# Kernel tuning notes

Hardware: AMD Instinct MI355X
Metric: run time of the kernel (lower is better)

Reference implementation:

```python
import jax, jax.numpy as jnp
import numpy as np
from jax import lax

NUM_CLASSES = 5  # config['training']['num_classes_per_task']
EMBED_DIM = 64


def _conv(x, w, b, pad):
    y = lax.conv_general_dilated(x, w, (1, 1), [(pad, pad), (pad, pad)],
                                 dimension_numbers=('NCHW', 'OIHW', 'NCHW'))
    return y + b[None, :, None, None]


def _maxpool2(x):
    n, c, h, w = x.shape
    return x.reshape(n, c, h // 2, 2, w // 2, 2).max(axis=(3, 5))


def _lenet(x, c1w, c1b, c2w, c2b, f1w, f1b, f2w, f2b, f3w, f3b):
    h = _maxpool2(jax.nn.relu(_conv(x, c1w, c1b, pad=2)))   # [N,6,14,14]
    h = _maxpool2(jax.nn.relu(_conv(h, c2w, c2b, pad=0)))   # [N,16,5,5]
    h = h.reshape(h.shape[0], -1)                            # [N,400]
    h = jax.nn.relu(h @ f1w.T + f1b)                         # [N,120]
    h = jax.nn.relu(h @ f2w.T + f2b)                         # [N,84]
    return h @ f3w.T + f3b                                   # [N,64]


def setup_inputs() -> dict:
    key = jax.random.key(0)
    ks = jax.random.split(key, 12)
    s = 0.1
    return {
        'x': jax.random.normal(ks[0], (20480, 1, 28, 28), dtype=jnp.float32),
        'c1w': jax.random.normal(ks[1], (6, 1, 5, 5), dtype=jnp.float32) * s,
        'c1b': jnp.zeros((6,), dtype=jnp.float32),
        'c2w': jax.random.normal(ks[2], (16, 6, 5, 5), dtype=jnp.float32) * s,
        'c2b': jnp.zeros((16,), dtype=jnp.float32),
        'f1w': jax.random.normal(ks[3], (120, 400), dtype=jnp.float32) * s,
        'f1b': jnp.zeros((120,), dtype=jnp.float32),
        'f2w': jax.random.normal(ks[4], (84, 120), dtype=jnp.float32) * s,
        'f2b': jnp.zeros((84,), dtype=jnp.float32),
        'f3w': jax.random.normal(ks[5], (EMBED_DIM, 84), dtype=jnp.float32) * s,
        'f3b': jnp.zeros((EMBED_DIM,), dtype=jnp.float32),
    }


def reference(x, c1w, c1b, c2w, c2b, f1w, f1b, f2w, f2b, f3w, f3b):
    emb = _lenet(x, c1w, c1b, c2w, c2b, f1w, f1b, f2w, f2b, f3w, f3b)  # [N,D]
    # Source builds a flat prototypes list of all N*D scalars / num_classes,
    # but only indices 0..D-1 are ever read -> first embedding row / num_classes.
    proto = emb[0] / NUM_CLASSES                     # [D]
    s = jax.nn.softmax(emb, axis=1)                  # softmax over dim 1
    # fun_L(x, p) = sqrt((x-p)^2) = |x-p|
    logits = jnp.abs(s - proto[None, :])             # [N,D]
    batch_size = x.shape[0] // NUM_CLASSES
    return logits.reshape(batch_size, NUM_CLASSES, -1)
```

## Files before the change

### kernel.cpp

```cpp
#include <hip/hip_runtime.h>


__device__ __forceinline__ int xcd_swizzle(int orig, int nwg) {
    int xcd = orig & 7, q = nwg >> 3, r = nwg & 7;
    int base = (xcd < r) ? xcd * (q + 1) : r * (q + 1) + (xcd - r) * q;
    return base + (orig >> 3);
}

__global__ __launch_bounds__(256) void transpose_x(
    const float* __restrict__ x, float* __restrict__ xt, int nc)
{
    __shared__ float t[64][65];
    const int tx = threadIdx.x & 63, ty = threadIdx.x >> 6;
    const int p0 = blockIdx.x * 64, n0 = blockIdx.y * 64;
    #pragma unroll
    for (int rr = 0; rr < 16; ++rr) {
        int nl = rr * 4 + ty;
        int pp = p0 + tx;
        int pr = pp >> 5, pc = pp & 31;
        float v = 0.f;
        if (pr >= 2 && pr < 30 && pc >= 2 && pc < 30)
            v = x[(size_t)(n0 + nl) * 784 + (pr - 2) * 28 + (pc - 2)];
        t[tx][nl] = v;
    }
    __syncthreads();
    #pragma unroll
    for (int rr = 0; rr < 16; ++rr) {
        int pl = rr * 4 + ty;
        xt[(size_t)(p0 + pl) * nc + n0 + tx] = t[pl][tx];
    }
}

__global__ __launch_bounds__(256, 2) void conv1_bt(
    const float* __restrict__ xt, const float* __restrict__ c1w,
    const float* __restrict__ c1b, float* __restrict__ p1t, int nc)
{
    const int newid = xcd_swizzle(blockIdx.x, gridDim.x);
    const int grp = newid / 392, rem = newid - grp * 392;
    const int pass = rem / 196, pos = rem - pass * 196;
    const int py = pos / 14, px = pos - py * 14;
    const int img = grp * 512 + threadIdx.x * 2;
    const float* pb = xt + (size_t)((2 * py) * 32 + 2 * px) * nc + img;

    float2 acc[12];
    #pragma unroll
    for (int i = 0; i < 12; ++i) acc[i] = make_float2(0.f, 0.f);

    #pragma unroll
    for (int r = 0; r < 6; ++r) {
        float2 row[6];
        #pragma unroll
        for (int cc = 0; cc < 6; ++cc)
            row[cc] = *(const float2*)&pb[(size_t)(r * 32 + cc) * nc];
        #pragma unroll
        for (int c3 = 0; c3 < 3; ++c3) {
            const float* wp = c1w + (pass * 3 + c3) * 25;
            if (r <= 4) {
                #pragma unroll
                for (int kx = 0; kx < 5; ++kx) {
                    float w = wp[r * 5 + kx];
                    acc[c3*4+0].x += row[kx].x   * w;
                    acc[c3*4+0].y += row[kx].y   * w;
                    acc[c3*4+1].x += row[kx+1].x * w;
                    acc[c3*4+1].y += row[kx+1].y * w;
                }
            }
            if (r >= 1) {
                #pragma unroll
                for (int kx = 0; kx < 5; ++kx) {
                    float w = wp[(r - 1) * 5 + kx];
                    acc[c3*4+2].x += row[kx].x   * w;
                    acc[c3*4+2].y += row[kx].y   * w;
                    acc[c3*4+3].x += row[kx+1].x * w;
                    acc[c3*4+3].y += row[kx+1].y * w;
                }
            }
        }
    }
    #pragma unroll
    for (int c3 = 0; c3 < 3; ++c3) {
        int ch = pass * 3 + c3;
        float b = c1b[ch];
        float mx = fmaxf(fmaxf(acc[c3*4+0].x, acc[c3*4+1].x),
                         fmaxf(acc[c3*4+2].x, acc[c3*4+3].x)) + b;
        float my = fmaxf(fmaxf(acc[c3*4+0].y, acc[c3*4+1].y),
                         fmaxf(acc[c3*4+2].y, acc[c3*4+3].y)) + b;
        float2 o2 = make_float2(fmaxf(mx, 0.f), fmaxf(my, 0.f));
        *(float2*)&p1t[(size_t)(ch * 196 + pos) * nc + img] = o2;
    }
}

__global__ __launch_bounds__(256, 2) void conv2_bt(
    const float* __restrict__ p1t, const float* __restrict__ c2w,
    const float* __restrict__ c2b, float* __restrict__ ht, int nc)
{
    const int newid = xcd_swizzle(blockIdx.x, gridDim.x);
    const int grp = newid / 100, rem = newid - grp * 100;
    const int pass = rem / 25, pos = rem - pass * 25;
    const int qy = pos / 5, qx = pos - qy * 5;
    const int img = grp * 512 + threadIdx.x * 2;
    const int y0 = 2 * qy, x0 = 2 * qx;

    float2 acc[16];
    #pragma unroll
    for (int i = 0; i < 16; ++i) acc[i] = make_float2(0.f, 0.f);

    #pragma unroll 1
    for (int ci = 0; ci < 6; ++ci) {
        const float* pb = p1t + (size_t)(ci * 196 + y0 * 14 + x0) * nc + img;
        #pragma unroll
        for (int r = 0; r < 6; ++r) {
            float2 row[6];
            #pragma unroll
            for (int cc = 0; cc < 6; ++cc)
                row[cc] = *(const float2*)&pb[(size_t)(r * 14 + cc) * nc];
            #pragma unroll
            for (int o4 = 0; o4 < 4; ++o4) {
                const float* wp = c2w + ((pass * 4 + o4) * 6 + ci) * 25;
                if (r <= 4) {
                    #pragma unroll
                    for (int kx = 0; kx < 5; ++kx) {
                        float w = wp[r * 5 + kx];
                        acc[o4*4+0].x += row[kx].x   * w;
                        acc[o4*4+0].y += row[kx].y   * w;
                        acc[o4*4+1].x += row[kx+1].x * w;
                        acc[o4*4+1].y += row[kx+1].y * w;
                    }
                }
                if (r >= 1) {
                    #pragma unroll
                    for (int kx = 0; kx < 5; ++kx) {
                        float w = wp[(r - 1) * 5 + kx];
                        acc[o4*4+2].x += row[kx].x   * w;
                        acc[o4*4+2].y += row[kx].y   * w;
                        acc[o4*4+3].x += row[kx+1].x * w;
                        acc[o4*4+3].y += row[kx+1].y * w;
                    }
                }
            }
        }
    }
    #pragma unroll
    for (int o4 = 0; o4 < 4; ++o4) {
        int oc = pass * 4 + o4;
        float b = c2b[oc];
        float mx = fmaxf(fmaxf(acc[o4*4+0].x, acc[o4*4+1].x),
                         fmaxf(acc[o4*4+2].x, acc[o4*4+3].x)) + b;
        float my = fmaxf(fmaxf(acc[o4*4+0].y, acc[o4*4+1].y),
                         fmaxf(acc[o4*4+2].y, acc[o4*4+3].y)) + b;
        float2 o2 = make_float2(fmaxf(mx, 0.f), fmaxf(my, 0.f));
        *(float2*)&ht[(size_t)(oc * 25 + pos) * nc + img] = o2;
    }
}

__global__ __launch_bounds__(256) void fc1_bt(
    const float* __restrict__ ht, const float* __restrict__ f1w,
    const float* __restrict__ f1b, float* __restrict__ a1t, int nc)
{
    const int newid = xcd_swizzle(blockIdx.x, gridDim.x);
    const int grp = newid / 15, og = newid - grp * 15;
    const int img = grp * 512 + threadIdx.x * 2;
    const float* wb = f1w + og * 8 * 400;

    float2 acc[8];
    #pragma unroll
    for (int j = 0; j < 8; ++j) acc[j] = make_float2(0.f, 0.f);

    #pragma unroll 4
    for (int k = 0; k < 400; ++k) {
        float2 hv = *(const float2*)&ht[(size_t)k * nc + img];
        #pragma unroll
        for (int j = 0; j < 8; ++j) {
            float w = wb[j * 400 + k];
            acc[j].x += hv.x * w;
            acc[j].y += hv.y * w;
        }
    }
    #pragma unroll
    for (int j = 0; j < 8; ++j) {
        int o = og * 8 + j;
        float b = f1b[o];
        float2 o2 = make_float2(fmaxf(acc[j].x + b, 0.f),
                                fmaxf(acc[j].y + b, 0.f));
        *(float2*)&a1t[(size_t)o * nc + img] = o2;
    }
}

__global__ __launch_bounds__(256) void fc2_bt(
    const float* __restrict__ a1t, const float* __restrict__ f2w,
    const float* __restrict__ f2b, float* __restrict__ a2t, int nc)
{
    const int newid = xcd_swizzle(blockIdx.x, gridDim.x);
    const int grp = newid / 12, og = newid - grp * 12;
    const int img = grp * 512 + threadIdx.x * 2;
    const float* wb = f2w + og * 7 * 120;

    float2 acc[7];
    #pragma unroll
    for (int j = 0; j < 7; ++j) acc[j] = make_float2(0.f, 0.f);

    #pragma unroll 4
    for (int k = 0; k < 120; ++k) {
        float2 hv = *(const float2*)&a1t[(size_t)k * nc + img];
        #pragma unroll
        for (int j = 0; j < 7; ++j) {
            float w = wb[j * 120 + k];
            acc[j].x += hv.x * w;
            acc[j].y += hv.y * w;
        }
    }
    #pragma unroll
    for (int j = 0; j < 7; ++j) {
        int o = og * 7 + j;
        float b = f2b[o];
        float2 o2 = make_float2(fmaxf(acc[j].x + b, 0.f),
                                fmaxf(acc[j].y + b, 0.f));
        *(float2*)&a2t[(size_t)o * nc + img] = o2;
    }
}

__global__ __launch_bounds__(256) void fc3_bt(
    const float* __restrict__ a2t, const float* __restrict__ f3w,
    const float* __restrict__ f3b, float* __restrict__ embt,
    int nc, int Ntot, int n0)
{
    const int newid = xcd_swizzle(blockIdx.x, gridDim.x);
    const int grp = newid / 8, og = newid - grp * 8;
    const int limg = grp * 512 + threadIdx.x * 2;
    const float* wb = f3w + og * 8 * 84;

    float2 acc[8];
    #pragma unroll
    for (int j = 0; j < 8; ++j) acc[j] = make_float2(0.f, 0.f);

    #pragma unroll 4
    for (int k = 0; k < 84; ++k) {
        float2 hv = *(const float2*)&a2t[(size_t)k * nc + limg];
        #pragma unroll
        for (int j = 0; j < 8; ++j) {
            float w = wb[j * 84 + k];
            acc[j].x += hv.x * w;
            acc[j].y += hv.y * w;
        }
    }
    #pragma unroll
    for (int j = 0; j < 8; ++j) {
        int o = og * 8 + j;
        float b = f3b[o];
        float2 o2 = make_float2(acc[j].x + b, acc[j].y + b);
        *(float2*)&embt[(size_t)o * Ntot + n0 + limg] = o2;
    }
}

__global__ __launch_bounds__(256) void proto_head_t(
    const float* __restrict__ embt, float* __restrict__ out, int N)
{
    const int img = blockIdx.x * 256 + threadIdx.x;
    float v[64];
    float m = -1e30f;
    #pragma unroll
    for (int o = 0; o < 64; ++o) {
        v[o] = embt[(size_t)o * N + img];
        m = fmaxf(m, v[o]);
    }
    float s = 0.f;
    #pragma unroll
    for (int o = 0; o < 64; ++o) {
        v[o] = __expf(v[o] - m);
        s += v[o];
    }
    float inv = __frcp_rn(s);
    #pragma unroll
    for (int o = 0; o < 64; o += 4) {
        float4 r;
        r.x = fabsf(v[o+0] * inv - embt[(size_t)(o+0) * N] * 0.2f);
        r.y = fabsf(v[o+1] * inv - embt[(size_t)(o+1) * N] * 0.2f);
        r.z = fabsf(v[o+2] * inv - embt[(size_t)(o+2) * N] * 0.2f);
        r.w = fabsf(v[o+3] * inv - embt[(size_t)(o+3) * N] * 0.2f);
        *(float4*)&out[(size_t)img * 64 + o] = r;
    }
}

extern "C" void kernel_launch(void* const* d_in, const int* in_sizes, int n_in,
                              void* d_out, int out_size, void* d_ws, size_t ws_size,
                              hipStream_t stream)
{
    const float* x   = (const float*)d_in[0];
    const float* c1w = (const float*)d_in[1];
    const float* c1b = (const float*)d_in[2];
    const float* c2w = (const float*)d_in[3];
    const float* c2b = (const float*)d_in[4];
    const float* f1w = (const float*)d_in[5];
    const float* f1b = (const float*)d_in[6];
    const float* f2w = (const float*)d_in[7];
    const float* f2b = (const float*)d_in[8];
    const float* f3w = (const float*)d_in[9];
    const float* f3b = (const float*)d_in[10];
    float* out = (float*)d_out;

    const int N = in_sizes[0] / 784;
    float* base = (float*)d_ws;

    int c = 40;
    const int cands[] = {1, 2, 4, 5, 8, 10, 20, 40};
    for (int k = 0; k < 8; ++k) {
        int cd = cands[k];
        if (N % cd) continue;
        int ncq = N / cd;
        if (ncq % 512) continue;
        size_t need = (size_t)8800 * ncq + (size_t)256 * N;
        if (need <= ws_size) { c = cd; break; }
    }
    const int nc = N / c;

    float* xt   = base;
    float* p1t  = base + (size_t)1024 * nc;
    float* ht_  = base;
    float* a1t  = p1t;
    float* a2t  = p1t + (size_t)120 * nc;
    float* embt = base + (size_t)2200 * nc;

    for (int k = 0; k < c; ++k) {
        int n0 = k * nc;
        transpose_x<<<dim3(16, nc / 64), 256, 0, stream>>>(
            x + (size_t)n0 * 784, xt, nc);
        conv1_bt<<<392 * (nc / 512), 256, 0, stream>>>(
            xt, c1w, c1b, p1t, nc);
        conv2_bt<<<100 * (nc / 512), 256, 0, stream>>>(
            p1t, c2w, c2b, ht_, nc);
        fc1_bt<<<15 * (nc / 512), 256, 0, stream>>>(
            ht_, f1w, f1b, a1t, nc);
        fc2_bt<<<12 * (nc / 512), 256, 0, stream>>>(
            a1t, f2w, f2b, a2t, nc);
        fc3_bt<<<8 * (nc / 512), 256, 0, stream>>>(
            a2t, f3w, f3b, embt, nc, N, n0);
    }
    proto_head_t<<<N / 256, 256, 0, stream>>>(embt, out, N);
}
```

Measured before the change: 299.4 us.

## Run conv2 on bf16 MFMA with hi/lo split-precision packing of activations

Conv1 now writes its output as packed bf16 hi/lo pairs in one 32-bit word per value. Conv2 is rewritten as an implicit GEMM on 16x16x32 bf16 MFMA instructions, using three products (hi*hi, hi*lo, lo*hi) to recover near-fp32 accuracy. The aim is to move conv2's scalar FMA work onto the matrix cores. In exchange, the B operand is gathered with scattered 32-bit loads per lane, and the result carries a small precision risk compared with fp32.

```diff
diff --git a/kernel.cpp b/kernel.cpp
--- a/kernel.cpp
+++ b/kernel.cpp
@@ -1,10 +1,22 @@
 #include <hip/hip_runtime.h>
 
+
+typedef __attribute__((ext_vector_type(8))) short bf16x8;
+typedef __attribute__((ext_vector_type(4))) float f32x4;
+
+union PackB { uint32_t u[4]; bf16x8 v; };
 
 __device__ __forceinline__ int xcd_swizzle(int orig, int nwg) {
     int xcd = orig & 7, q = nwg >> 3, r = nwg & 7;
     int base = (xcd < r) ? xcd * (q + 1) : r * (q + 1) + (xcd - r) * q;
     return base + (orig >> 3);
+}
+
+__device__ __forceinline__ uint32_t pack_hilo(float v) {
+    uint32_t u = __float_as_uint(v);
+    uint32_t hb = u & 0xFFFF0000u;
+    float lo = v - __uint_as_float(hb);
+    return hb | (__float_as_uint(lo) >> 16);
 }
 
 __global__ __launch_bounds__(256) void transpose_x(
@@ -33,7 +45,7 @@
 
 __global__ __launch_bounds__(256, 2) void conv1_bt(
     const float* __restrict__ xt, const float* __restrict__ c1w,
-    const float* __restrict__ c1b, float* __restrict__ p1t, int nc)
+    const float* __restrict__ c1b, uint32_t* __restrict__ p1p, int nc)
 {
     const int newid = xcd_swizzle(blockIdx.x, gridDim.x);
     const int grp = newid / 392, rem = newid - grp * 392;
@@ -85,71 +97,97 @@
                          fmaxf(acc[c3*4+2].x, acc[c3*4+3].x)) + b;
         float my = fmaxf(fmaxf(acc[c3*4+0].y, acc[c3*4+1].y),
                          fmaxf(acc[c3*4+2].y, acc[c3*4+3].y)) + b;
-        float2 o2 = make_float2(fmaxf(mx, 0.f), fmaxf(my, 0.f));
-        *(float2*)&p1t[(size_t)(ch * 196 + pos) * nc + img] = o2;
-    }
-}
-
-__global__ __launch_bounds__(256, 2) void conv2_bt(
-    const float* __restrict__ p1t, const float* __restrict__ c2w,
+        uint2 o2;
+        o2.x = pack_hilo(fmaxf(mx, 0.f));
+        o2.y = pack_hilo(fmaxf(my, 0.f));
+        *(uint2*)&p1p[(size_t)(ch * 196 + pos) * nc + img] = o2;
+    }
+}
+
+__global__ __launch_bounds__(256) void conv2_mfma(
+    const uint32_t* __restrict__ p1p, const float* __restrict__ c2w,
     const float* __restrict__ c2b, float* __restrict__ ht, int nc)
 {
     const int newid = xcd_swizzle(blockIdx.x, gridDim.x);
-    const int grp = newid / 100, rem = newid - grp * 100;
-    const int pass = rem / 25, pos = rem - pass * 25;
+    const int grp = newid / 25, pos = newid - grp * 25;
     const int qy = pos / 5, qx = pos - qy * 5;
-    const int img = grp * 512 + threadIdx.x * 2;
-    const int y0 = 2 * qy, x0 = 2 * qx;
-
-    float2 acc[16];
-    #pragma unroll
-    for (int i = 0; i < 16; ++i) acc[i] = make_float2(0.f, 0.f);
-
+    const int wave = threadIdx.x >> 6, lane = threadIdx.x & 63;
+    const int lhi = lane >> 4, llo = lane & 15;
+
+    uint32_t voff[5][8];
+    bf16x8 wh[5], wl[5];
+    #pragma unroll
+    for (int s = 0; s < 5; ++s) {
+        PackB ph, pl;
+        #pragma unroll
+        for (int j = 0; j < 8; ++j) {
+            int k = s * 32 + lhi * 8 + j;
+            int kc = (k < 150) ? k : 149;
+            int ci = kc / 25, r = kc - ci * 25;
+            int ky = r / 5, kx = r - ky * 5;
+            int feat0 = ci * 196 + (2 * qy + ky) * 14 + (2 * qx + kx);
+            voff[s][j] = (uint32_t)feat0 * (uint32_t)nc + wave * 16 + llo;
+            float w = (k < 150) ? c2w[(llo * 6 + ci) * 25 + r] : 0.f;
+            uint32_t u  = __float_as_uint(w);
+            uint32_t hb = u & 0xFFFF0000u;
+            float    lo = w - __uint_as_float(hb);
+            uint32_t lb = __float_as_uint(lo) & 0xFFFF0000u;
+            if (j & 1) { ph.u[j >> 1] |= hb;       pl.u[j >> 1] |= lb; }
+            else       { ph.u[j >> 1]  = hb >> 16; pl.u[j >> 1]  = lb >> 16; }
+        }
+        wh[s] = ph.v; wl[s] = pl.v;
+    }
+    float bias[4];
+    size_t rowoff[4];
+    #pragma unroll
+    for (int r = 0; r < 4; ++r) {
+        int oc = lhi * 4 + r;
+        bias[r] = c2b[oc];
+        rowoff[r] = (size_t)(oc * 25 + pos) * nc;
+    }
+
+    const int imgbase = grp * 256;
     #pragma unroll 1
-    for (int ci = 0; ci < 6; ++ci) {
-        const float* pb = p1t + (size_t)(ci * 196 + y0 * 14 + x0) * nc + img;
-        #pragma unroll
-        for (int r = 0; r < 6; ++r) {
-            float2 row[6];
+    for (int it = 0; it < 4; ++it) {
+        f32x4 acc[4];
+        #pragma unroll
+        for (int p = 0; p < 4; ++p) acc[p] = (f32x4)(0.f);
+
+        #pragma unroll
+        for (int s = 0; s < 5; ++s) {
             #pragma unroll
-            for (int cc = 0; cc < 6; ++cc)
-                row[cc] = *(const float2*)&pb[(size_t)(r * 14 + cc) * nc];
-            #pragma unroll
-            for (int o4 = 0; o4 < 4; ++o4) {
-                const float* wp = c2w + ((pass * 4 + o4) * 6 + ci) * 25;
-                if (r <= 4) {
-                    #pragma unroll
-                    for (int kx = 0; kx < 5; ++kx) {
-                        float w = wp[r * 5 + kx];
-                        acc[o4*4+0].x += row[kx].x   * w;
-                        acc[o4*4+0].y += row[kx].y   * w;
-                        acc[o4*4+1].x += row[kx+1].x * w;
-                        acc[o4*4+1].y += row[kx+1].y * w;
-                    }
-                }
-                if (r >= 1) {
-                    #pragma unroll
-                    for (int kx = 0; kx < 5; ++kx) {
-                        float w = wp[(r - 1) * 5 + kx];
-                        acc[o4*4+2].x += row[kx].x   * w;
-                        acc[o4*4+2].y += row[kx].y   * w;
-                        acc[o4*4+3].x += row[kx+1].x * w;
-                        acc[o4*4+3].y += row[kx+1].y * w;
-                    }
-                }
+            for (int p = 0; p < 4; ++p) {
+                const uint32_t* ptr =
+                    p1p + (size_t)((p >> 1) * 14 + (p & 1)) * nc
+                        + imgbase + it * 64;
+                uint32_t w0 = ptr[voff[s][0]], w1 = ptr[voff[s][1]];
+                uint32_t w2 = ptr[voff[s][2]], w3 = ptr[voff[s][3]];
+                uint32_t w4 = ptr[voff[s][4]], w5 = ptr[voff[s][5]];
+                uint32_t w6 = ptr[voff[s][6]], w7 = ptr[voff[s][7]];
+                PackB bh, bl;
+                bh.u[0] = (w0 >> 16) | (w1 & 0xFFFF0000u);
+                bh.u[1] = (w2 >> 16) | (w3 & 0xFFFF0000u);
+                bh.u[2] = (w4 >> 16) | (w5 & 0xFFFF0000u);
+                bh.u[3] = (w6 >> 16) | (w7 & 0xFFFF0000u);
+                bl.u[0] = (w0 & 0xFFFFu) | (w1 << 16);
+                bl.u[1] = (w2 & 0xFFFFu) | (w3 << 16);
+                bl.u[2] = (w4 & 0xFFFFu) | (w5 << 16);
+                bl.u[3] = (w6 & 0xFFFFu) | (w7 << 16);
+                acc[p] = __builtin_amdgcn_mfma_f32_16x16x32_bf16(
+                             wh[s], bh.v, acc[p], 0, 0, 0);
+                acc[p] = __builtin_amdgcn_mfma_f32_16x16x32_bf16(
+                             wh[s], bl.v, acc[p], 0, 0, 0);
+                acc[p] = __builtin_amdgcn_mfma_f32_16x16x32_bf16(
+                             wl[s], bh.v, acc[p], 0, 0, 0);
             }
         }
-    }
-    #pragma unroll
-    for (int o4 = 0; o4 < 4; ++o4) {
-        int oc = pass * 4 + o4;
-        float b = c2b[oc];
-        float mx = fmaxf(fmaxf(acc[o4*4+0].x, acc[o4*4+1].x),
-                         fmaxf(acc[o4*4+2].x, acc[o4*4+3].x)) + b;
-        float my = fmaxf(fmaxf(acc[o4*4+0].y, acc[o4*4+1].y),
-                         fmaxf(acc[o4*4+2].y, acc[o4*4+3].y)) + b;
-        float2 o2 = make_float2(fmaxf(mx, 0.f), fmaxf(my, 0.f));
-        *(float2*)&ht[(size_t)(oc * 25 + pos) * nc + img] = o2;
+        #pragma unroll
+        for (int r = 0; r < 4; ++r) {
+            float m = fmaxf(fmaxf(acc[0][r], acc[1][r]),
+                            fmaxf(acc[2][r], acc[3][r]));
+            m = fmaxf(m + bias[r], 0.f);
+            ht[rowoff[r] + imgbase + it * 64 + wave * 16 + llo] = m;
+        }
     }
 }
 
@@ -313,21 +351,21 @@
     }
     const int nc = N / c;
 
-    float* xt   = base;
-    float* p1t  = base + (size_t)1024 * nc;
-    float* ht_  = base;
-    float* a1t  = p1t;
-    float* a2t  = p1t + (size_t)120 * nc;
-    float* embt = base + (size_t)2200 * nc;
+    float*    xt   = base;
+    uint32_t* p1p  = (uint32_t*)(base + (size_t)1024 * nc);
+    float*    ht_  = base;
+    float*    a1t  = (float*)p1p;
+    float*    a2t  = (float*)p1p + (size_t)120 * nc;
+    float*    embt = base + (size_t)2200 * nc;
 
     for (int k = 0; k < c; ++k) {
         int n0 = k * nc;
         transpose_x<<<dim3(16, nc / 64), 256, 0, stream>>>(
             x + (size_t)n0 * 784, xt, nc);
         conv1_bt<<<392 * (nc / 512), 256, 0, stream>>>(
-            xt, c1w, c1b, p1t, nc);
-        conv2_bt<<<100 * (nc / 512), 256, 0, stream>>>(
-            p1t, c2w, c2b, ht_, nc);
+            xt, c1w, c1b, p1p, nc);
+        conv2_mfma<<<25 * (nc / 256), 256, 0, stream>>>(
+            p1p, c2w, c2b, ht_, nc);
         fc1_bt<<<15 * (nc / 512), 256, 0, stream>>>(
             ht_, f1w, f1b, a1t, nc);
         fc2_bt<<<12 * (nc / 512), 256, 0, stream>>>(
```

Result: slower. 412.9 us (+37.9%).
